# Kernel tuning notes

Measured on AMD Instinct MI355X. Metric: run time of the kernel, lower is better.

The kernel has to match this reference:

```python
import jax, jax.numpy as jnp
import numpy as np

N_NODES = 100000
N_EDGES = 1200000
D_IN = 64
D_HID = 64
D_OUT = 32


def setup_inputs() -> dict:
    key = jax.random.key(0)
    ks = jax.random.split(key, 8)
    x = jax.random.normal(ks[0], (N_NODES, D_IN), dtype=jnp.float32)
    edge_index = jax.random.randint(ks[1], (2, N_EDGES), 0, N_NODES, dtype=jnp.int64)
    s = 0.05
    W1 = jax.random.normal(ks[2], (D_IN, D_HID), dtype=jnp.float32) * s
    b1 = jnp.zeros((D_HID,), dtype=jnp.float32)
    W2 = jax.random.normal(ks[3], (D_HID, D_HID), dtype=jnp.float32) * s
    b2 = jnp.zeros((D_HID,), dtype=jnp.float32)
    Wl = jax.random.normal(ks[4], (D_HID, D_OUT), dtype=jnp.float32) * s
    bl = jax.random.normal(ks[5], (D_OUT,), dtype=jnp.float32) * s
    return {"x": x, "edge_index": edge_index, "W1": W1, "b1": b1,
            "W2": W2, "b2": b2, "Wl": Wl, "bl": bl}


def reference(x, edge_index, W1, b1, W2, b2, Wl, bl):
    n = x.shape[0]
    # PyG GCNConv default: add self-loops, symmetric normalization D^-1/2 (A+I) D^-1/2
    loops = jnp.arange(n, dtype=edge_index.dtype)
    src = jnp.concatenate([edge_index[0], loops])  # message sources
    dst = jnp.concatenate([edge_index[1], loops])  # aggregation targets
    deg = jax.ops.segment_sum(jnp.ones(dst.shape, x.dtype), dst, num_segments=n)
    dinv = jax.lax.rsqrt(deg)  # deg >= 1 due to self-loops
    norm = dinv[src] * dinv[dst]  # [E+N]

    def gcn_conv(h, W, b):
        h = h @ W                      # transform [N, d]
        m = h[src] * norm[:, None]     # gather + scale [E+N, d]
        return jax.ops.segment_sum(m, dst, num_segments=n) + b  # scatter-add

    h = jax.nn.relu(gcn_conv(x, W1, b1))
    h = jax.nn.relu(gcn_conv(h, W2, b2))
    return h @ Wl + bl
```

## Files before the change

### kernel.cpp

```cpp
#include <hip/hip_runtime.h>
#include <hip/hip_fp16.h>

#define N_NODES 100000
#define N_EDGES 1200000

#define BIN_SHIFT 6
#define NODES_PER_BIN 64
#define NBINS ((N_NODES + NODES_PER_BIN - 1) >> BIN_SHIFT)
#define CAP 1024
#define EPB 4096
#define NBLK_BIN ((N_EDGES + EPB - 1) / EPB)

__global__ void zero_int_kernel(int* __restrict__ p, int n) {
    int i = blockIdx.x * blockDim.x + threadIdx.x;
    if (i < n) p[i] = 0;
}

__global__ void binning_kernel(const int* __restrict__ src, const int* __restrict__ dst,
                               int* __restrict__ gcursor, unsigned int* __restrict__ binned,
                               int E) {
    __shared__ unsigned int stage[EPB];
    __shared__ unsigned short sbin[EPB];
    __shared__ unsigned int hist[NBINS];
    int t = threadIdx.x;
    int e_base = blockIdx.x * EPB;

    for (int b = t; b < NBINS; b += 256) hist[b] = 0;
    __syncthreads();

#pragma unroll
    for (int j = 0; j < EPB / 256; ++j) {
        int idx = e_base + t + j * 256;
        if (idx < E) {
            int s = src[idx];
            int d = dst[idx];
            unsigned int bin = (unsigned int)d >> BIN_SHIFT;
            stage[t + j * 256] = (unsigned int)s | (((unsigned int)d & 63u) << 17);
            sbin[t + j * 256] = (unsigned short)bin;
            atomicAdd(&hist[bin], 1u);
        }
    }
    __syncthreads();

    for (int b = t; b < NBINS; b += 256) {
        unsigned int c = hist[b];
        if (c) hist[b] = (unsigned int)(b * CAP) + (unsigned int)atomicAdd(&gcursor[b], (int)c);
    }
    __syncthreads();

#pragma unroll
    for (int j = 0; j < EPB / 256; ++j) {
        int idx = e_base + t + j * 256;
        if (idx < E) {
            unsigned int bin = sbin[t + j * 256];
            unsigned int pos = atomicAdd(&hist[bin], 1u);
            binned[pos] = stage[t + j * 256];
        }
    }
}

__global__ void dinv_kernel(const unsigned int* __restrict__ binned,
                            const int* __restrict__ gcursor,
                            float* __restrict__ dinv) {
    __shared__ unsigned int counts[NODES_PER_BIN];
    int bin = blockIdx.x;
    int t = threadIdx.x;
    if (t < NODES_PER_BIN) counts[t] = 0;
    __syncthreads();
    int nb = gcursor[bin];
    const unsigned int* eb = binned + (size_t)bin * CAP;
    for (int i = t; i < nb; i += 256) atomicAdd(&counts[eb[i] >> 17], 1u);
    __syncthreads();
    if (t < NODES_PER_BIN) {
        int node = bin * NODES_PER_BIN + t;
        if (node < N_NODES) dinv[node] = rsqrtf((float)(counts[t] + 1u));
    }
}

template<int DOUT, bool HALF_OUT>
__global__ __launch_bounds__(256, 4) void gemm_kernel(const float* __restrict__ X,
                                                      const float* __restrict__ W,
                                                      const float* __restrict__ bias,
                                                      const float* __restrict__ rowscale,
                                                      void* __restrict__ Hout, int n) {
    constexpr int COLG = DOUT / 4;
    constexpr int RGS  = 256 / COLG;
    constexpr int RPT  = 64 / RGS;
    constexpr int XPITCH = 17;
    __shared__ float4 sW4[64 * COLG];
    __shared__ float4 sX4[64 * XPITCH];
    int tid = threadIdx.x;

    for (int i = tid; i < 64 * COLG; i += 256) sW4[i] = ((const float4*)W)[i];

    int base_row = blockIdx.x * 64;
    const float4* X4 = (const float4*)X;
    for (int i = tid; i < 64 * 16; i += 256) {
        int r = i >> 4, c = i & 15;
        int gr = base_row + r;
        float4 v = make_float4(0.f, 0.f, 0.f, 0.f);
        if (gr < n) v = X4[(size_t)gr * 16 + c];
        sX4[r * XPITCH + c] = v;
    }
    __syncthreads();

    int cg = tid % COLG;
    int rg = tid / COLG;
    float4 acc[RPT];
#pragma unroll
    for (int r = 0; r < RPT; ++r) acc[r] = make_float4(0.f, 0.f, 0.f, 0.f);

#pragma unroll 2
    for (int k4 = 0; k4 < 16; ++k4) {
        float4 xv[RPT];
#pragma unroll
        for (int r = 0; r < RPT; ++r) xv[r] = sX4[(rg + RGS * r) * XPITCH + k4];
#pragma unroll
        for (int kk = 0; kk < 4; ++kk) {
            float4 w = sW4[(k4 * 4 + kk) * COLG + cg];
#pragma unroll
            for (int r = 0; r < RPT; ++r) {
                float xs = (kk == 0) ? xv[r].x : (kk == 1) ? xv[r].y : (kk == 2) ? xv[r].z : xv[r].w;
                acc[r].x = fmaf(xs, w.x, acc[r].x);
                acc[r].y = fmaf(xs, w.y, acc[r].y);
                acc[r].z = fmaf(xs, w.z, acc[r].z);
                acc[r].w = fmaf(xs, w.w, acc[r].w);
            }
        }
    }

#pragma unroll
    for (int r = 0; r < RPT; ++r) {
        int grow = base_row + rg + RGS * r;
        if (grow < n) {
            float4 v = acc[r];
            if (rowscale) {
                float s = rowscale[grow];
                v.x *= s; v.y *= s; v.z *= s; v.w *= s;
            }
            if (bias) {
                float4 bb = ((const float4*)bias)[cg];
                v.x += bb.x; v.y += bb.y; v.z += bb.z; v.w += bb.w;
            }
            if (HALF_OUT) {
                __half2* H2 = (__half2*)Hout;
                size_t idx = (size_t)grow * (DOUT / 2) + 2 * cg;
                H2[idx]     = __floats2half2_rn(v.x, v.y);
                H2[idx + 1] = __floats2half2_rn(v.z, v.w);
            } else {
                ((float4*)Hout)[(size_t)grow * COLG + cg] = v;
            }
        }
    }
}

__global__ void aggregate_kernel(const __half* __restrict__ tmp,
                                 const unsigned int* __restrict__ binned,
                                 const int* __restrict__ gcursor,
                                 const float* __restrict__ dinv,
                                 const float* __restrict__ b,
                                 float* __restrict__ h) {
    __shared__ unsigned int eLDS[CAP];
    __shared__ unsigned int srcs[CAP];
    __shared__ unsigned int counts[NODES_PER_BIN];
    __shared__ unsigned int scan[NODES_PER_BIN];
    __shared__ unsigned int offs[NODES_PER_BIN];
    __shared__ unsigned int cur[NODES_PER_BIN];
    int bin = blockIdx.x;
    int t = threadIdx.x;
    int nb = gcursor[bin];
    const unsigned int* eb = binned + (size_t)bin * CAP;

    if (t < NODES_PER_BIN) counts[t] = 0;
    __syncthreads();
    for (int i = t; i < nb; i += 256) {
        unsigned int p = eb[i];
        eLDS[i] = p;
        atomicAdd(&counts[p >> 17], 1u);
    }
    __syncthreads();
    if (t < NODES_PER_BIN) scan[t] = counts[t];
    __syncthreads();
    for (int step = 1; step < NODES_PER_BIN; step <<= 1) {
        unsigned int v = 0;
        if (t < NODES_PER_BIN && t >= step) v = scan[t - step];
        __syncthreads();
        if (t < NODES_PER_BIN) scan[t] += v;
        __syncthreads();
    }
    if (t < NODES_PER_BIN) {
        offs[t] = scan[t] - counts[t];
        cur[t] = 0;
    }
    __syncthreads();
    for (int i = t; i < nb; i += 256) {
        unsigned int p = eLDS[i];
        unsigned int l = p >> 17;
        unsigned int pos = offs[l] + atomicAdd(&cur[l], 1u);
        srcs[pos] = p & 0x1FFFFu;
    }
    __syncthreads();

    int oct = t & 7;
    int lnode0 = t >> 3;
    const uint4* tmp16 = (const uint4*)tmp;
    float bb[8];
    {
        const float4 b0 = ((const float4*)b)[oct * 2];
        const float4 b1 = ((const float4*)b)[oct * 2 + 1];
        bb[0] = b0.x; bb[1] = b0.y; bb[2] = b0.z; bb[3] = b0.w;
        bb[4] = b1.x; bb[5] = b1.y; bb[6] = b1.z; bb[7] = b1.w;
    }

#pragma unroll
    for (int g = 0; g < 2; ++g) {
        int ln = g * 32 + lnode0;
        int node = bin * NODES_PER_BIN + ln;
        if (node < N_NODES) {
            int deg = (int)counts[ln];
            int beg = (int)offs[ln];
            float acc[8];
            {
                uint4 raw = tmp16[(size_t)node * 8 + oct];
                const __half2* hp = (const __half2*)&raw;
#pragma unroll
                for (int j = 0; j < 4; ++j) {
                    float2 f = __half22float2(hp[j]);
                    acc[2 * j] = f.x; acc[2 * j + 1] = f.y;
                }
            }
            int e = 0;
            for (; e + 3 < deg; e += 4) {
                unsigned int s0 = srcs[beg + e];
                unsigned int s1 = srcs[beg + e + 1];
                unsigned int s2 = srcs[beg + e + 2];
                unsigned int s3 = srcs[beg + e + 3];
                uint4 r0 = tmp16[(size_t)s0 * 8 + oct];
                uint4 r1 = tmp16[(size_t)s1 * 8 + oct];
                uint4 r2 = tmp16[(size_t)s2 * 8 + oct];
                uint4 r3 = tmp16[(size_t)s3 * 8 + oct];
                const __half2* h0 = (const __half2*)&r0;
                const __half2* h1 = (const __half2*)&r1;
                const __half2* h2 = (const __half2*)&r2;
                const __half2* h3 = (const __half2*)&r3;
#pragma unroll
                for (int j = 0; j < 4; ++j) {
                    float2 f0 = __half22float2(h0[j]);
                    float2 f1 = __half22float2(h1[j]);
                    float2 f2 = __half22float2(h2[j]);
                    float2 f3 = __half22float2(h3[j]);
                    acc[2 * j]     += (f0.x + f1.x) + (f2.x + f3.x);
                    acc[2 * j + 1] += (f0.y + f1.y) + (f2.y + f3.y);
                }
            }
            for (; e < deg; ++e) {
                unsigned int s0 = srcs[beg + e];
                uint4 r0 = tmp16[(size_t)s0 * 8 + oct];
                const __half2* h0 = (const __half2*)&r0;
#pragma unroll
                for (int j = 0; j < 4; ++j) {
                    float2 f0 = __half22float2(h0[j]);
                    acc[2 * j]     += f0.x;
                    acc[2 * j + 1] += f0.y;
                }
            }
            float dv = dinv[node];
            float4 o0, o1;
            o0.x = fmaxf(fmaf(dv, acc[0], bb[0]), 0.0f);
            o0.y = fmaxf(fmaf(dv, acc[1], bb[1]), 0.0f);
            o0.z = fmaxf(fmaf(dv, acc[2], bb[2]), 0.0f);
            o0.w = fmaxf(fmaf(dv, acc[3], bb[3]), 0.0f);
            o1.x = fmaxf(fmaf(dv, acc[4], bb[4]), 0.0f);
            o1.y = fmaxf(fmaf(dv, acc[5], bb[5]), 0.0f);
            o1.z = fmaxf(fmaf(dv, acc[6], bb[6]), 0.0f);
            o1.w = fmaxf(fmaf(dv, acc[7], bb[7]), 0.0f);
            float4* hv = (float4*)(h + (size_t)node * 64 + oct * 8);
            hv[0] = o0;
            hv[1] = o1;
        }
    }
}

extern "C" void kernel_launch(void* const* d_in, const int* in_sizes, int n_in,
                              void* d_out, int out_size, void* d_ws, size_t ws_size,
                              hipStream_t stream) {
    const float* x  = (const float*)d_in[0];
    const int*   ei = (const int*)d_in[1];
    const float* W1 = (const float*)d_in[2];
    const float* b1 = (const float*)d_in[3];
    const float* W2 = (const float*)d_in[4];
    const float* b2 = (const float*)d_in[5];
    const float* Wl = (const float*)d_in[6];
    const float* bl = (const float*)d_in[7];
    float* out = (float*)d_out;

    const int N = N_NODES;
    const int E = N_EDGES;
    const int* src = ei;
    const int* dst = ei + E;

    char* ws = (char*)d_ws;
    size_t off = 0;
    auto align = [](size_t v) { return (v + 511) & ~(size_t)511; };
    int* gcursor         = (int*)(ws + off);          off = align(off + (size_t)NBINS * 4);
    float* dinv          = (float*)(ws + off);        off = align(off + (size_t)N * 4);
    unsigned int* binned = (unsigned int*)(ws + off); off = align(off + (size_t)NBINS * CAP * 4);
    __half* tmp          = (__half*)(ws + off);       off = align(off + (size_t)N * 64 * 2);
    float* h             = (float*)(ws + off);        off = align(off + (size_t)N * 64 * 4);
    (void)ws_size;

    const int NBLK_GEMM = (N + 63) / 64;

    zero_int_kernel<<<(NBINS + 255) / 256, 256, 0, stream>>>(gcursor, NBINS);
    binning_kernel<<<NBLK_BIN, 256, 0, stream>>>(src, dst, gcursor, binned, E);
    dinv_kernel<<<NBINS, 256, 0, stream>>>(binned, gcursor, dinv);

    gemm_kernel<64, true><<<NBLK_GEMM, 256, 0, stream>>>(x, W1, nullptr, dinv, tmp, N);
    aggregate_kernel<<<NBINS, 256, 0, stream>>>(tmp, binned, gcursor, dinv, b1, h);

    gemm_kernel<64, true><<<NBLK_GEMM, 256, 0, stream>>>(h, W2, nullptr, dinv, tmp, N);
    aggregate_kernel<<<NBINS, 256, 0, stream>>>(tmp, binned, gcursor, dinv, b2, h);

    gemm_kernel<32, false><<<NBLK_GEMM, 256, 0, stream>>>(h, Wl, bl, nullptr, out, N);
}
```

Measured before the change: 215.7 us.

## Build per-bin CSR once and reuse it in both aggregation passes

The degree kernel becomes a CSR-building kernel. It sorts each bin's edges by destination in place and stores a packed offset/degree per node. The two aggregation kernels then just copy the sorted sources into LDS instead of redoing the histogram, scan and scatter every time. The change also swaps the zero kernel for hipMemsetAsync and doubles edges per binning block, which means fewer blocks each doing more work.

Result: no change. 219.9 us (+2.0%).

```diff
diff --git a/kernel.cpp b/kernel.cpp
--- a/kernel.cpp
+++ b/kernel.cpp
@@ -8,13 +8,8 @@
 #define NODES_PER_BIN 64
 #define NBINS ((N_NODES + NODES_PER_BIN - 1) >> BIN_SHIFT)
 #define CAP 1024
-#define EPB 4096
+#define EPB 8192
 #define NBLK_BIN ((N_EDGES + EPB - 1) / EPB)
-
-__global__ void zero_int_kernel(int* __restrict__ p, int n) {
-    int i = blockIdx.x * blockDim.x + threadIdx.x;
-    if (i < n) p[i] = 0;
-}
 
 __global__ void binning_kernel(const int* __restrict__ src, const int* __restrict__ dst,
                                int* __restrict__ gcursor, unsigned int* __restrict__ binned,
@@ -59,21 +54,54 @@
     }
 }
 
-__global__ void dinv_kernel(const unsigned int* __restrict__ binned,
-                            const int* __restrict__ gcursor,
-                            float* __restrict__ dinv) {
+__global__ void csr_kernel(unsigned int* __restrict__ binned,
+                           const int* __restrict__ gcursor,
+                           float* __restrict__ dinv,
+                           unsigned int* __restrict__ offdeg) {
+    __shared__ unsigned int eLDS[CAP];
     __shared__ unsigned int counts[NODES_PER_BIN];
+    __shared__ unsigned int scan[NODES_PER_BIN];
+    __shared__ unsigned int offs[NODES_PER_BIN];
+    __shared__ unsigned int cur[NODES_PER_BIN];
     int bin = blockIdx.x;
     int t = threadIdx.x;
+    int nb = gcursor[bin];
+    unsigned int* eb = binned + (size_t)bin * CAP;
+
     if (t < NODES_PER_BIN) counts[t] = 0;
     __syncthreads();
-    int nb = gcursor[bin];
-    const unsigned int* eb = binned + (size_t)bin * CAP;
-    for (int i = t; i < nb; i += 256) atomicAdd(&counts[eb[i] >> 17], 1u);
-    __syncthreads();
+    for (int i = t; i < nb; i += 256) {
+        unsigned int p = eb[i];
+        eLDS[i] = p;
+        atomicAdd(&counts[p >> 17], 1u);
+    }
+    __syncthreads();
+    if (t < NODES_PER_BIN) scan[t] = counts[t];
+    __syncthreads();
+    for (int step = 1; step < NODES_PER_BIN; step <<= 1) {
+        unsigned int v = 0;
+        if (t < NODES_PER_BIN && t >= step) v = scan[t - step];
+        __syncthreads();
+        if (t < NODES_PER_BIN) scan[t] += v;
+        __syncthreads();
+    }
+    if (t < NODES_PER_BIN) {
+        offs[t] = scan[t] - counts[t];
+        cur[t] = 0;
+    }
+    __syncthreads();
+    for (int i = t; i < nb; i += 256) {
+        unsigned int p = eLDS[i];
+        unsigned int l = p >> 17;
+        unsigned int pos = offs[l] + atomicAdd(&cur[l], 1u);
+        eb[pos] = p & 0x1FFFFu;
+    }
     if (t < NODES_PER_BIN) {
         int node = bin * NODES_PER_BIN + t;
-        if (node < N_NODES) dinv[node] = rsqrtf((float)(counts[t] + 1u));
+        if (node < N_NODES) {
+            dinv[node] = rsqrtf((float)(counts[t] + 1u));
+            offdeg[node] = (offs[t] << 16) | counts[t];
+        }
     }
 }
 
@@ -157,48 +185,24 @@
 __global__ void aggregate_kernel(const __half* __restrict__ tmp,
                                  const unsigned int* __restrict__ binned,
                                  const int* __restrict__ gcursor,
+                                 const unsigned int* __restrict__ offdeg,
                                  const float* __restrict__ dinv,
                                  const float* __restrict__ b,
                                  float* __restrict__ h) {
-    __shared__ unsigned int eLDS[CAP];
     __shared__ unsigned int srcs[CAP];
-    __shared__ unsigned int counts[NODES_PER_BIN];
-    __shared__ unsigned int scan[NODES_PER_BIN];
-    __shared__ unsigned int offs[NODES_PER_BIN];
-    __shared__ unsigned int cur[NODES_PER_BIN];
+    __shared__ unsigned int sOffdeg[NODES_PER_BIN];
+    __shared__ float sDinv[NODES_PER_BIN];
     int bin = blockIdx.x;
     int t = threadIdx.x;
     int nb = gcursor[bin];
     const unsigned int* eb = binned + (size_t)bin * CAP;
 
-    if (t < NODES_PER_BIN) counts[t] = 0;
-    __syncthreads();
-    for (int i = t; i < nb; i += 256) {
-        unsigned int p = eb[i];
-        eLDS[i] = p;
-        atomicAdd(&counts[p >> 17], 1u);
-    }
-    __syncthreads();
-    if (t < NODES_PER_BIN) scan[t] = counts[t];
-    __syncthreads();
-    for (int step = 1; step < NODES_PER_BIN; step <<= 1) {
-        unsigned int v = 0;
-        if (t < NODES_PER_BIN && t >= step) v = scan[t - step];
-        __syncthreads();
-        if (t < NODES_PER_BIN) scan[t] += v;
-        __syncthreads();
-    }
     if (t < NODES_PER_BIN) {
-        offs[t] = scan[t] - counts[t];
-        cur[t] = 0;
-    }
-    __syncthreads();
-    for (int i = t; i < nb; i += 256) {
-        unsigned int p = eLDS[i];
-        unsigned int l = p >> 17;
-        unsigned int pos = offs[l] + atomicAdd(&cur[l], 1u);
-        srcs[pos] = p & 0x1FFFFu;
-    }
+        int node = bin * NODES_PER_BIN + t;
+        sOffdeg[t] = (node < N_NODES) ? offdeg[node] : 0;
+        sDinv[t] = (node < N_NODES) ? dinv[node] : 0.0f;
+    }
+    for (int i = t; i < nb; i += 256) srcs[i] = eb[i];
     __syncthreads();
 
     int oct = t & 7;
@@ -217,8 +221,9 @@
         int ln = g * 32 + lnode0;
         int node = bin * NODES_PER_BIN + ln;
         if (node < N_NODES) {
-            int deg = (int)counts[ln];
-            int beg = (int)offs[ln];
+            unsigned int od = sOffdeg[ln];
+            int deg = (int)(od & 0xFFFFu);
+            int beg = (int)(od >> 16);
             float acc[8];
             {
                 uint4 raw = tmp16[(size_t)node * 8 + oct];
@@ -264,7 +269,7 @@
                     acc[2 * j + 1] += f0.y;
                 }
             }
-            float dv = dinv[node];
+            float dv = sDinv[ln];
             float4 o0, o1;
             o0.x = fmaxf(fmaf(dv, acc[0], bb[0]), 0.0f);
             o0.y = fmaxf(fmaf(dv, acc[1], bb[1]), 0.0f);
@@ -304,6 +309,7 @@
     auto align = [](size_t v) { return (v + 511) & ~(size_t)511; };
     int* gcursor         = (int*)(ws + off);          off = align(off + (size_t)NBINS * 4);
     float* dinv          = (float*)(ws + off);        off = align(off + (size_t)N * 4);
+    unsigned int* offdeg = (unsigned int*)(ws + off); off = align(off + (size_t)N * 4);
     unsigned int* binned = (unsigned int*)(ws + off); off = align(off + (size_t)NBINS * CAP * 4);
     __half* tmp          = (__half*)(ws + off);       off = align(off + (size_t)N * 64 * 2);
     float* h             = (float*)(ws + off);        off = align(off + (size_t)N * 64 * 4);
@@ -311,15 +317,15 @@
 
     const int NBLK_GEMM = (N + 63) / 64;
 
-    zero_int_kernel<<<(NBINS + 255) / 256, 256, 0, stream>>>(gcursor, NBINS);
+    hipMemsetAsync(gcursor, 0, (size_t)NBINS * 4, stream);
     binning_kernel<<<NBLK_BIN, 256, 0, stream>>>(src, dst, gcursor, binned, E);
-    dinv_kernel<<<NBINS, 256, 0, stream>>>(binned, gcursor, dinv);
+    csr_kernel<<<NBINS, 256, 0, stream>>>(binned, gcursor, dinv, offdeg);
 
     gemm_kernel<64, true><<<NBLK_GEMM, 256, 0, stream>>>(x, W1, nullptr, dinv, tmp, N);
-    aggregate_kernel<<<NBINS, 256, 0, stream>>>(tmp, binned, gcursor, dinv, b1, h);
+    aggregate_kernel<<<NBINS, 256, 0, stream>>>(tmp, binned, gcursor, offdeg, dinv, b1, h);
 
     gemm_kernel<64, true><<<NBLK_GEMM, 256, 0, stream>>>(h, W2, nullptr, dinv, tmp, N);
-    aggregate_kernel<<<NBINS, 256, 0, stream>>>(tmp, binned, gcursor, dinv, b2, h);
+    aggregate_kernel<<<NBINS, 256, 0, stream>>>(tmp, binned, gcursor, offdeg, b2 ? dinv : dinv, b2, h);
 
     gemm_kernel<32, false><<<NBLK_GEMM, 256, 0, stream>>>(h, Wl, bl, nullptr, out, N);
 }
```
